# Kernel tuning notes

Hardware: AMD Instinct MI355X
Metric: run time of the kernel (lower is better)

## Reference

```python
import jax, jax.numpy as jnp
import numpy as np
import math

H, W = 32, 32
HEAD = 8
ZONE = 2
D_MODEL = 512
BT, N, C = 8, H * W, D_MODEL
T = 4


def setup_inputs() -> dict:
    key = jax.random.key(0)
    ks = jax.random.split(key, 9)
    s = 1.0 / math.sqrt(D_MODEL)
    inp = {
        "x": jax.random.normal(ks[0], (BT, N, C), dtype=jnp.float32),
        "t": T,
        "Wq": jax.random.normal(ks[1], (C, C), dtype=jnp.float32) * s,
        "bq": jnp.zeros((C,), dtype=jnp.float32),
        "Wk": jax.random.normal(ks[2], (C, C), dtype=jnp.float32) * s,
        "bk": jnp.zeros((C,), dtype=jnp.float32),
        "Wv": jax.random.normal(ks[3], (C, C), dtype=jnp.float32) * s,
        "bv": jnp.zeros((C,), dtype=jnp.float32),
        "Wo": jax.random.normal(ks[4], (C, C), dtype=jnp.float32) * s,
        "bo": jnp.zeros((C,), dtype=jnp.float32),
    }
    return inp


def _to_windows(y, b, t, c_h):
    # [bt, n, c] -> [b, zone^2, head, t*(h/z)*(w/z), c_h]
    y = y.reshape(b, t, ZONE, H // ZONE, ZONE, W // ZONE, HEAD, c_h)
    y = jnp.transpose(y, (0, 2, 4, 6, 1, 3, 5, 7))
    return y.reshape(b, ZONE * ZONE, HEAD, -1, c_h)


def reference(x, t, Wq, bq, Wk, bk, Wv, bv, Wo, bo):
    bt, n, c = x.shape
    b = bt // t
    c_h = c // HEAD
    q = x @ Wq.T + bq
    k = x @ Wk.T + bk
    v = x @ Wv.T + bv
    q = _to_windows(q, b, t, c_h)  # [b, z^2, head, L, c_h]
    k = _to_windows(k, b, t, c_h)
    v = _to_windows(v, b, t, c_h)
    scores = jnp.einsum('bzhlc,bzhmc->bzhlm', q, k) / math.sqrt(c_h)
    p = jax.nn.softmax(scores, axis=-1)
    att = jnp.einsum('bzhlm,bzhmc->bzhlc', p, v)  # [b, z^2, head, L, c_h]
    att = att.reshape(b, ZONE, ZONE, HEAD, t, H // ZONE, W // ZONE, c_h)
    att = jnp.transpose(att, (0, 4, 1, 5, 2, 6, 3, 7)).reshape(bt, n, c)
    return att @ Wo.T + bo
```

## Files before the change

kernel.cpp:

```cpp
#include <hip/hip_runtime.h>
#include <math.h>
#include <stdint.h>


typedef unsigned short u16;
typedef unsigned int u32;
typedef __attribute__((ext_vector_type(8))) short bf16x8;
typedef __attribute__((ext_vector_type(4))) float f32x4;
typedef __attribute__((ext_vector_type(16))) float f32x16;

__device__ __forceinline__ u16 f2b(float f) {
  u32 u = __float_as_uint(f);
  return (u16)((u + 0x7FFFu + ((u >> 16) & 1u)) >> 16);
}

__device__ __forceinline__ void gld_lds16(const void* g, void* l) {
  auto gp = (__attribute__((address_space(1))) u32*)(uintptr_t)g;
  auto lp = (__attribute__((address_space(3))) u32*)(u32)(uintptr_t)l;
  __builtin_amdgcn_global_load_lds(gp, lp, 16, 0, 0);
}

__global__ __launch_bounds__(256)
void prep_cvt(const float* __restrict__ x, const float* __restrict__ wq,
              const float* __restrict__ wk, const float* __restrict__ wv,
              const float* __restrict__ wo, u16* __restrict__ xb,
              u16* __restrict__ wqb, u16* __restrict__ wkb,
              u16* __restrict__ wvb, u16* __restrict__ wob)
{
  int i = blockIdx.x * 256 + threadIdx.x;
  const float* src; u16* dst; int off;
  if (i < 1048576) { src = x; dst = xb; off = i; }
  else {
    int j = i - 1048576; int w = j >> 16; off = j & 65535;
    src = (w == 0) ? wq : (w == 1) ? wk : (w == 2) ? wv : wo;
    dst = (w == 0) ? wqb : (w == 1) ? wkb : (w == 2) ? wvb : wob;
  }
  float4 v = ((const float4*)src)[off];
  ushort4 o;
  o.x = f2b(v.x); o.y = f2b(v.y); o.z = f2b(v.z); o.w = f2b(v.w);
  ((ushort4*)dst)[off] = o;
}

__global__ __launch_bounds__(256, 2)
void gemm_qkv(const u16* __restrict__ A, const u16* __restrict__ Bq,
              const u16* __restrict__ Bk, const u16* __restrict__ Bv,
              const float* __restrict__ bq, const float* __restrict__ bk,
              const float* __restrict__ bv, u16* __restrict__ qw,
              u16* __restrict__ kw, u16* __restrict__ vt)
{
  __shared__ u16 As[2][8192];
  __shared__ u16 Ws[3][2][4096];
  const int tid = threadIdx.x;
  const int lane = tid & 63;
  const int wbase = (tid & 192) * 8;
  const int m0 = blockIdx.y * 128, n0 = blockIdx.x * 64;
  const int wm = ((tid >> 7) & 1) * 64;
  const int wn = ((tid >> 6) & 1) * 32;
  const int arow = tid >> 3, aslot = tid & 7;

  f32x4 accq[4][2], acck[4][2], accv[4][2];
#pragma unroll
  for (int i = 0; i < 4; ++i)
#pragma unroll
    for (int j = 0; j < 2; ++j) {
#pragma unroll
      for (int r = 0; r < 4; ++r) { accq[i][j][r] = 0.f; acck[i][j][r] = 0.f; accv[i][j][r] = 0.f; }
    }

  auto stage = [&](int t, int buf) {
#pragma unroll
    for (int q = 0; q < 4; ++q) {
      int row = q * 32 + arow;
      int sl = aslot ^ (row & 7);
      gld_lds16(A + (size_t)(m0 + row) * 512 + t * 64 + sl * 8,
                &As[buf][q * 2048 + wbase]);
    }
    const u16* bp[3] = {Bq, Bk, Bv};
#pragma unroll
    for (int w = 0; w < 3; ++w)
#pragma unroll
      for (int q = 0; q < 2; ++q) {
        int row = q * 32 + arow;
        int sl = aslot ^ (row & 7);
        gld_lds16(bp[w] + (size_t)(n0 + row) * 512 + t * 64 + sl * 8,
                  &Ws[w][buf][q * 2048 + wbase]);
      }
  };

  stage(0, 0);
  __syncthreads();
  int cur = 0;
#pragma unroll 1
  for (int t = 0; t < 8; ++t) {
    if (t < 7) stage(t + 1, cur ^ 1);
    const u16* la = As[cur];
    bf16x8 af[4][2];
#pragma unroll
    for (int mf = 0; mf < 4; ++mf)
#pragma unroll
      for (int ks = 0; ks < 2; ++ks) {
        int row = wm + mf * 16 + (lane & 15);
        int s = ks * 4 + (lane >> 4);
        af[mf][ks] = *(const bf16x8*)(la + row * 64 + ((s ^ (row & 7)) << 3));
      }
    __builtin_amdgcn_s_setprio(1);
#pragma unroll
    for (int ks = 0; ks < 2; ++ks)
#pragma unroll
      for (int nf = 0; nf < 2; ++nf) {
        int row = wn + nf * 16 + (lane & 15);
        int s = ks * 4 + (lane >> 4);
        int boff = row * 64 + ((s ^ (row & 7)) << 3);
        bf16x8 bq8 = *(const bf16x8*)(Ws[0][cur] + boff);
        bf16x8 bk8 = *(const bf16x8*)(Ws[1][cur] + boff);
        bf16x8 bv8 = *(const bf16x8*)(Ws[2][cur] + boff);
#pragma unroll
        for (int mf = 0; mf < 4; ++mf) {
          accq[mf][nf] = __builtin_amdgcn_mfma_f32_16x16x32_bf16(af[mf][ks], bq8, accq[mf][nf], 0, 0, 0);
          acck[mf][nf] = __builtin_amdgcn_mfma_f32_16x16x32_bf16(af[mf][ks], bk8, acck[mf][nf], 0, 0, 0);
          accv[mf][nf] = __builtin_amdgcn_mfma_f32_16x16x32_bf16(af[mf][ks], bv8, accv[mf][nf], 0, 0, 0);
        }
      }
    __builtin_amdgcn_s_setprio(0);
    __syncthreads();
    cur ^= 1;
  }

  int h[2], d[2]; float bqv[2], bkv[2], bvv[2];
#pragma unroll
  for (int nf = 0; nf < 2; ++nf) {
    int col = n0 + wn + nf * 16 + (lane & 15);
    h[nf] = col >> 6; d[nf] = col & 63;
    bqv[nf] = bq[col]; bkv[nf] = bk[col]; bvv[nf] = bv[col];
  }
#pragma unroll
  for (int mf = 0; mf < 4; ++mf) {
    int mb = m0 + wm + mf * 16 + ((lane >> 4) << 2);
    int b = mb >> 12, t = (mb >> 10) & 3, row32 = (mb >> 5) & 31, col32 = mb & 31;
    int zi = row32 >> 4, hirow = row32 & 15, zj = col32 >> 4, wj = col32 & 15;
    int gb = b * 32 + (zi * 2 + zj) * 8;
    int l0 = t * 256 + hirow * 16 + wj;
#pragma unroll
    for (int nf = 0; nf < 2; ++nf) {
      size_t qkbase = ((size_t)(gb + h[nf]) * 1024 + l0) * 64 + d[nf];
#pragma unroll
      for (int r = 0; r < 4; ++r) {
        qw[qkbase + (size_t)r * 64] = f2b(accq[mf][nf][r] + bqv[nf]);
        kw[qkbase + (size_t)r * 64] = f2b(acck[mf][nf][r] + bkv[nf]);
      }
      ushort4 pv;
      pv.x = f2b(accv[mf][nf][0] + bvv[nf]);
      pv.y = f2b(accv[mf][nf][1] + bvv[nf]);
      pv.z = f2b(accv[mf][nf][2] + bvv[nf]);
      pv.w = f2b(accv[mf][nf][3] + bvv[nf]);
      *(ushort4*)(vt + ((size_t)(gb + h[nf]) * 64 + d[nf]) * 1024 + l0) = pv;
    }
  }
}

__global__ __launch_bounds__(256, 2)
void attn32(const u16* __restrict__ qw, const u16* __restrict__ kw,
            const u16* __restrict__ vt, u16* __restrict__ attb)
{
  __shared__ u16 Kl[2][2][4096];
  __shared__ u16 Vl[2][2][4096];

  const int tid = threadIdx.x, lane = tid & 63, wid = tid >> 6;
  const int hi = lane >> 5, ln = lane & 31;
  const int n = blockIdx.x;
  const int work = (n & 7) * 64 + (n >> 3);
  const int g = work >> 3, qt = work & 7;
  const int b = g >> 5, z = (g >> 3) & 3, h = g & 7, zi = z >> 1, zj = z & 1;
  const u16* qg = qw + (size_t)g * 65536;
  const u16* kg = kw + (size_t)g * 65536;
  const u16* vg = vt + (size_t)g * 65536;
  const int q0 = qt * 128 + wid * 32;
  const float SC2 = 0.125f * 1.44269504089f;
  const float SHIFT = -20.f;

  const int t8 = lane >> 3, s8 = lane & 7;

  auto stageKV = [&](int c, int pb, int hf) {
#pragma unroll
    for (int p = 0; p < 2; ++p) {
      int row = wid * 16 + p * 8 + t8;
      gld_lds16(kg + (size_t)(c * 64 + row) * 64 + ((s8 ^ (row & 7)) << 3),
                Kl[pb][hf] + wid * 1024 + p * 512);
      gld_lds16(vg + (size_t)row * 1024 + c * 64 + ((s8 ^ (row & 7)) << 3),
                Vl[pb][hf] + wid * 1024 + p * 512);
    }
  };

  bf16x8 qf[4];
#pragma unroll
  for (int ks = 0; ks < 4; ++ks)
    qf[ks] = *(const bf16x8*)(qg + (size_t)(q0 + ln) * 64 + ks * 16 + hi * 8);

  f32x16 o[2];
#pragma unroll
  for (int nf = 0; nf < 2; ++nf)
#pragma unroll
    for (int r = 0; r < 16; ++r) o[nf][r] = 0.f;
  float lrun = 0.f;

  auto qkt = [&](const u16* Kb, f32x16 (&st)[2]) {
    bf16x8 kk[2][4];
#pragma unroll
    for (int kb = 0; kb < 2; ++kb)
#pragma unroll
      for (int ks = 0; ks < 4; ++ks) {
        int row = kb * 32 + ln;
        int sl = (ks * 2 + hi) ^ (ln & 7);
        kk[kb][ks] = *(const bf16x8*)(Kb + row * 64 + sl * 8);
      }
#pragma unroll
    for (int kb = 0; kb < 2; ++kb)
#pragma unroll
      for (int r = 0; r < 16; ++r) st[kb][r] = 0.f;
    __builtin_amdgcn_s_setprio(1);
#pragma unroll
    for (int ks = 0; ks < 4; ++ks) {
      st[0] = __builtin_amdgcn_mfma_f32_32x32x16_bf16(kk[0][ks], qf[ks], st[0], 0, 0, 0);
      st[1] = __builtin_amdgcn_mfma_f32_32x32x16_bf16(kk[1][ks], qf[ks], st[1], 0, 0, 0);
    }
    __builtin_amdgcn_s_setprio(0);
  };

  auto softmax_pv = [&](f32x16 (&st)[2], const u16* Vb) -> float {
    float racc[4] = {0.f, 0.f, 0.f, 0.f};
#pragma unroll
    for (int kb = 0; kb < 2; ++kb)
#pragma unroll
      for (int r = 0; r < 16; ++r) {
        float p = exp2f(fmaf(st[kb][r], SC2, SHIFT));
        st[kb][r] = p;
        racc[r & 3] += p;
      }
    u32 W[2][4][2];
#pragma unroll
    for (int kb = 0; kb < 2; ++kb)
#pragma unroll
      for (int j = 0; j < 4; ++j)
#pragma unroll
        for (int u = 0; u < 2; ++u) {
          u32 w;
          asm("v_cvt_pk_bf16_f32 %0, %1, %2"
              : "=v"(w) : "v"(st[kb][4 * j + 2 * u]), "v"(st[kb][4 * j + 2 * u + 1]));
          W[kb][j][u] = w;
        }
    __builtin_amdgcn_s_setprio(1);
#pragma unroll
    for (int ks = 0; ks < 4; ++ks) {
      const int kb = ks >> 1, sl2 = ks & 1;
      u32 a0 = W[kb][2 * sl2][0], b0 = W[kb][2 * sl2 + 1][0];
      u32 a1 = W[kb][2 * sl2][1], b1 = W[kb][2 * sl2 + 1][1];
      asm volatile("v_permlane32_swap_b32 %0, %1" : "+v"(a0), "+v"(b0));
      asm volatile("v_permlane32_swap_b32 %0, %1" : "+v"(a1), "+v"(b1));
      union { u32 u[4]; bf16x8 v; } pu;
      pu.u[0] = a0; pu.u[1] = a1; pu.u[2] = b0; pu.u[3] = b1;
#pragma unroll
      for (int nf = 0; nf < 2; ++nf) {
        int drow = nf * 32 + ln;
        int vsl = (ks * 2 + hi) ^ (ln & 7);
        bf16x8 vf = *(const bf16x8*)(Vb + drow * 64 + vsl * 8);
        o[nf] = __builtin_amdgcn_mfma_f32_32x32x16_bf16(pu.v, vf, o[nf], 0, 0, 0);
      }
    }
    __builtin_amdgcn_s_setprio(0);
    return (racc[0] + racc[1]) + (racc[2] + racc[3]);
  };

  stageKV(0, 0, 0);
  stageKV(1, 0, 1);
  asm volatile("s_waitcnt vmcnt(0)" ::: "memory");
  __builtin_amdgcn_s_barrier();
  __builtin_amdgcn_sched_barrier(0);

#pragma unroll 1
  for (int cp = 0; cp < 8; ++cp) {
    const int pb = cp & 1;
    if (cp < 7) { stageKV(2 * cp + 2, pb ^ 1, 0); stageKV(2 * cp + 3, pb ^ 1, 1); }

    f32x16 stA[2], stB[2];
    qkt(Kl[pb][0], stA);
    qkt(Kl[pb][1], stB);
    float rsA = softmax_pv(stA, Vl[pb][0]);
    float rsB = softmax_pv(stB, Vl[pb][1]);
    float rs = rsA + rsB;
    rs += __shfl_xor(rs, 32);
    lrun += rs;

    if (cp < 7) {
      asm volatile("s_waitcnt vmcnt(0)" ::: "memory");
      __builtin_amdgcn_s_barrier();
      __builtin_amdgcn_sched_barrier(0);
    }
  }

  const int rowbase = b * 4096 + zi * 512 + zj * 16;
  const int colbase = h * 64;
#pragma unroll
  for (int r = 0; r < 16; ++r) {
    int qr = (r & 3) + 8 * (r >> 2) + 4 * hi;
    float lv = __shfl(lrun, qr);
    float iv = 1.f / lv;
    int l = q0 + qr;
    int row = rowbase + ((l >> 8) << 10) + (((l >> 4) & 15) << 5) + (l & 15);
    size_t off = (size_t)row * 512 + colbase + ln;
    attb[off] = f2b(o[0][r] * iv);
    attb[off + 32] = f2b(o[1][r] * iv);
  }
}

__global__ __launch_bounds__(256, 2)
void gemm_o(const u16* __restrict__ A, const u16* __restrict__ B,
            const float* __restrict__ bias, float* __restrict__ Cout)
{
  __shared__ u16 lds[2][12288];
  const int tid = threadIdx.x;
  const int lane = tid & 63;
  const int wbase = (tid & 192) * 8;
  const int m0 = blockIdx.y * 128, n0 = blockIdx.x * 64;
  const int wm = ((tid >> 7) & 1) * 64;
  const int wn = ((tid >> 6) & 1) * 32;
  const int arow = tid >> 3, aslot = tid & 7;

  f32x4 acc[4][2];
#pragma unroll
  for (int i = 0; i < 4; ++i)
#pragma unroll
    for (int j = 0; j < 2; ++j)
#pragma unroll
      for (int r = 0; r < 4; ++r) acc[i][j][r] = 0.f;

  auto stage = [&](int t, int buf) {
#pragma unroll
    for (int q = 0; q < 4; ++q) {
      int row = q * 32 + arow;
      int sl = aslot ^ (row & 7);
      gld_lds16(A + (size_t)(m0 + row) * 512 + t * 64 + sl * 8,
                &lds[buf][q * 2048 + wbase]);
    }
#pragma unroll
    for (int q = 0; q < 2; ++q) {
      int row = q * 32 + arow;
      int sl = aslot ^ (row & 7);
      gld_lds16(B + (size_t)(n0 + row) * 512 + t * 64 + sl * 8,
                &lds[buf][8192 + q * 2048 + wbase]);
    }
  };

  stage(0, 0);
  __syncthreads();
  int cur = 0;
#pragma unroll 1
  for (int t = 0; t < 8; ++t) {
    if (t < 7) stage(t + 1, cur ^ 1);
    const u16* la = lds[cur];
    const u16* lb = lds[cur] + 8192;
    bf16x8 af[4][2];
#pragma unroll
    for (int mf = 0; mf < 4; ++mf)
#pragma unroll
      for (int ks = 0; ks < 2; ++ks) {
        int row = wm + mf * 16 + (lane & 15);
        int s = ks * 4 + (lane >> 4);
        af[mf][ks] = *(const bf16x8*)(la + row * 64 + ((s ^ (row & 7)) << 3));
      }
    __builtin_amdgcn_s_setprio(1);
#pragma unroll
    for (int ks = 0; ks < 2; ++ks)
#pragma unroll
      for (int nf = 0; nf < 2; ++nf) {
        int row = wn + nf * 16 + (lane & 15);
        int s = ks * 4 + (lane >> 4);
        bf16x8 bfr = *(const bf16x8*)(lb + row * 64 + ((s ^ (row & 7)) << 3));
#pragma unroll
        for (int mf = 0; mf < 4; ++mf)
          acc[mf][nf] = __builtin_amdgcn_mfma_f32_16x16x32_bf16(af[mf][ks], bfr, acc[mf][nf], 0, 0, 0);
      }
    __builtin_amdgcn_s_setprio(0);
    __syncthreads();
    cur ^= 1;
  }

#pragma unroll
  for (int mf = 0; mf < 4; ++mf)
#pragma unroll
    for (int nf = 0; nf < 2; ++nf) {
      int row = m0 + wm + mf * 16 + ((lane >> 4) << 2);
      int col = n0 + wn + nf * 16 + (lane & 15);
      float bi = bias[col];
#pragma unroll
      for (int r = 0; r < 4; ++r)
        Cout[(size_t)(row + r) * 512 + col] = acc[mf][nf][r] + bi;
    }
}

extern "C" void kernel_launch(void* const* d_in, const int* in_sizes, int n_in,
                              void* d_out, int out_size, void* d_ws, size_t ws_size,
                              hipStream_t stream) {
  const float* x  = (const float*)d_in[0];
  const float* Wq = (const float*)d_in[2];
  const float* bq = (const float*)d_in[3];
  const float* Wk = (const float*)d_in[4];
  const float* bk = (const float*)d_in[5];
  const float* Wv = (const float*)d_in[6];
  const float* bv = (const float*)d_in[7];
  const float* Wo = (const float*)d_in[8];
  const float* bo = (const float*)d_in[9];

  u16* xb   = (u16*)d_ws;
  u16* wqb  = xb + 4194304;
  u16* wkb  = wqb + 262144;
  u16* wvb  = wkb + 262144;
  u16* wob  = wvb + 262144;
  u16* qwb  = wob + 262144;
  u16* kwb  = qwb + 4194304;
  u16* vtb  = kwb + 4194304;
  u16* attb = vtb + 4194304;

  prep_cvt<<<5120, 256, 0, stream>>>(x, Wq, Wk, Wv, Wo, xb, wqb, wkb, wvb, wob);
  gemm_qkv<<<dim3(8, 64), 256, 0, stream>>>(xb, wqb, wkb, wvb, bq, bk, bv, qwb, kwb, vtb);
  attn32<<<512, 256, 0, stream>>>(qwb, kwb, vtb, attb);
  gemm_o<<<dim3(8, 64), 256, 0, stream>>>(attb, wob, bo, (float*)d_out);
}
```

Baseline: 81.98 us.

## Fuse x fp32-to-bf16 conversion into QKV GEMM A-tile loading

Removes the separate conversion of x to bf16 (a 16MB read plus 8MB write pass) by having gemm_qkv load fp32 x tiles into registers, convert them with v_cvt_pk_bf16_f32, and write them swizzled into LDS after the compute of each stage. The prep kernel now only converts the weights. In exchange, each A tile is read in fp32 by the 8 column blocks, doubling A read traffic per block, and register pressure rises from holding 8 float4 prefetch values.

```diff
diff --git a/kernel.cpp b/kernel.cpp
--- a/kernel.cpp
+++ b/kernel.cpp
@@ -21,20 +21,15 @@
 }
 
 __global__ __launch_bounds__(256)
-void prep_cvt(const float* __restrict__ x, const float* __restrict__ wq,
-              const float* __restrict__ wk, const float* __restrict__ wv,
-              const float* __restrict__ wo, u16* __restrict__ xb,
-              u16* __restrict__ wqb, u16* __restrict__ wkb,
-              u16* __restrict__ wvb, u16* __restrict__ wob)
+void prep_w(const float* __restrict__ wq, const float* __restrict__ wk,
+            const float* __restrict__ wv, const float* __restrict__ wo,
+            u16* __restrict__ wqb, u16* __restrict__ wkb,
+            u16* __restrict__ wvb, u16* __restrict__ wob)
 {
   int i = blockIdx.x * 256 + threadIdx.x;
-  const float* src; u16* dst; int off;
-  if (i < 1048576) { src = x; dst = xb; off = i; }
-  else {
-    int j = i - 1048576; int w = j >> 16; off = j & 65535;
-    src = (w == 0) ? wq : (w == 1) ? wk : (w == 2) ? wv : wo;
-    dst = (w == 0) ? wqb : (w == 1) ? wkb : (w == 2) ? wvb : wob;
-  }
+  int w = i >> 16, off = i & 65535;
+  const float* src = (w == 0) ? wq : (w == 1) ? wk : (w == 2) ? wv : wo;
+  u16* dst = (w == 0) ? wqb : (w == 1) ? wkb : (w == 2) ? wvb : wob;
   float4 v = ((const float4*)src)[off];
   ushort4 o;
   o.x = f2b(v.x); o.y = f2b(v.y); o.z = f2b(v.z); o.w = f2b(v.w);
@@ -42,7 +37,7 @@
 }
 
 __global__ __launch_bounds__(256, 2)
-void gemm_qkv(const u16* __restrict__ A, const u16* __restrict__ Bq,
+void gemm_qkv(const float* __restrict__ X, const u16* __restrict__ Bq,
               const u16* __restrict__ Bk, const u16* __restrict__ Bv,
               const float* __restrict__ bq, const float* __restrict__ bk,
               const float* __restrict__ bv, u16* __restrict__ qw,
@@ -67,14 +62,29 @@
       for (int r = 0; r < 4; ++r) { accq[i][j][r] = 0.f; acck[i][j][r] = 0.f; accv[i][j][r] = 0.f; }
     }
 
-  auto stage = [&](int t, int buf) {
-#pragma unroll
-    for (int q = 0; q < 4; ++q) {
-      int row = q * 32 + arow;
-      int sl = aslot ^ (row & 7);
-      gld_lds16(A + (size_t)(m0 + row) * 512 + t * 64 + sl * 8,
-                &As[buf][q * 2048 + wbase]);
-    }
+  float4 ar[8];
+  auto loadA = [&](int t) {
+#pragma unroll
+    for (int i2 = 0; i2 < 8; ++i2) {
+      int idx = i2 * 256 + tid;
+      int row = idx >> 4, h16 = idx & 15;
+      ar[i2] = *(const float4*)(X + (size_t)(m0 + row) * 512 + t * 64 + h16 * 4);
+    }
+  };
+  auto writeA = [&](int buf) {
+#pragma unroll
+    for (int i2 = 0; i2 < 8; ++i2) {
+      int idx = i2 * 256 + tid;
+      int row = idx >> 4, h16 = idx & 15;
+      int slot = h16 >> 1, half = h16 & 1;
+      u32 lo, hi2;
+      asm("v_cvt_pk_bf16_f32 %0, %1, %2" : "=v"(lo) : "v"(ar[i2].x), "v"(ar[i2].y));
+      asm("v_cvt_pk_bf16_f32 %0, %1, %2" : "=v"(hi2) : "v"(ar[i2].z), "v"(ar[i2].w));
+      uint2 w2; w2.x = lo; w2.y = hi2;
+      *(uint2*)(&As[buf][row * 64 + ((slot ^ (row & 7)) << 3) + half * 4]) = w2;
+    }
+  };
+  auto stageB = [&](int t, int buf) {
     const u16* bp[3] = {Bq, Bk, Bv};
 #pragma unroll
     for (int w = 0; w < 3; ++w)
@@ -87,12 +97,14 @@
       }
   };
 
-  stage(0, 0);
+  loadA(0);
+  stageB(0, 0);
+  writeA(0);
   __syncthreads();
   int cur = 0;
 #pragma unroll 1
   for (int t = 0; t < 8; ++t) {
-    if (t < 7) stage(t + 1, cur ^ 1);
+    if (t < 7) { loadA(t + 1); stageB(t + 1, cur ^ 1); }
     const u16* la = As[cur];
     bf16x8 af[4][2];
 #pragma unroll
@@ -122,6 +134,7 @@
         }
       }
     __builtin_amdgcn_s_setprio(0);
+    if (t < 7) writeA(cur ^ 1);
     __syncthreads();
     cur ^= 1;
   }
@@ -410,8 +423,7 @@
   const float* Wo = (const float*)d_in[8];
   const float* bo = (const float*)d_in[9];
 
-  u16* xb   = (u16*)d_ws;
-  u16* wqb  = xb + 4194304;
+  u16* wqb  = (u16*)d_ws;
   u16* wkb  = wqb + 262144;
   u16* wvb  = wkb + 262144;
   u16* wob  = wvb + 262144;
@@ -420,8 +432,8 @@
   u16* vtb  = kwb + 4194304;
   u16* attb = vtb + 4194304;
 
-  prep_cvt<<<5120, 256, 0, stream>>>(x, Wq, Wk, Wv, Wo, xb, wqb, wkb, wvb, wob);
-  gemm_qkv<<<dim3(8, 64), 256, 0, stream>>>(xb, wqb, wkb, wvb, bq, bk, bv, qwb, kwb, vtb);
+  prep_w<<<1024, 256, 0, stream>>>(Wq, Wk, Wv, Wo, wqb, wkb, wvb, wob);
+  gemm_qkv<<<dim3(8, 64), 256, 0, stream>>>(x, wqb, wkb, wvb, bq, bk, bv, qwb, kwb, vtb);
   attn32<<<512, 256, 0, stream>>>(qwb, kwb, vtb, attb);
   gemm_o<<<dim3(8, 64), 256, 0, stream>>>(attb, wob, bo, (float*)d_out);
 }
```

Result: no change. 82.39 us (+0.5%).
